# Kernel optimization log

Measured on AMD Instinct MI355X. Metric: run time of the kernel, lower is better.

The kernel has to match this reference:

```python
import jax, jax.numpy as jnp
import numpy as np

H = 64
HD = H // 2
N_PACKET = 8192
N_ROUTER = 16384
N_CHANNEL = 65536
E_PASS = 65536
N_CLASSES = 11  # pred_exp_max - pred_exp_min
NUM_MP = 2


def setup_inputs() -> dict:
    key = jax.random.key(0)
    ks = iter(jax.random.split(key, 32))

    def W(shape):
        return jax.random.normal(next(ks), shape, dtype=jnp.float32) * 0.02

    inp = {}
    # node features
    inp["freq"] = jax.random.uniform(next(ks), (N_PACKET, 1), dtype=jnp.float32)
    inp["flit"] = jax.random.normal(next(ks), (N_PACKET, 32), dtype=jnp.float32)
    inp["op_type"] = jax.random.normal(next(ks), (N_ROUTER, 4), dtype=jnp.float32)
    inp["bandwidth"] = jax.random.uniform(next(ks), (N_CHANNEL, 1), dtype=jnp.float32)
    # hetero edges: 'output' router->channel, 'input' channel->router, 'pass' packet->channel
    inp["out_src"] = jax.random.randint(next(ks), (N_CHANNEL,), 0, N_ROUTER, dtype=jnp.int32)
    inp["out_dst"] = jnp.arange(N_CHANNEL, dtype=jnp.int32)
    inp["in_src"] = jnp.arange(N_CHANNEL, dtype=jnp.int32)
    inp["in_dst"] = jax.random.randint(next(ks), (N_CHANNEL,), 0, N_ROUTER, dtype=jnp.int32)
    inp["pass_src"] = jax.random.randint(next(ks), (E_PASS,), 0, N_PACKET, dtype=jnp.int32)
    inp["pass_dst"] = jax.random.randint(next(ks), (E_PASS,), 0, N_CHANNEL, dtype=jnp.int32)
    # FeatureGen params
    inp["w_freq"] = W((1, H)); inp["b_freq"] = jnp.zeros((H,), jnp.float32)
    inp["w_flit"] = W((32, H)); inp["b_flit"] = jnp.zeros((H,), jnp.float32)
    inp["w_op"] = W((4, H)); inp["b_op"] = jnp.zeros((H,), jnp.float32)
    inp["w_bw"] = W((1, H)); inp["b_bw"] = jnp.zeros((H,), jnp.float32)
    inp["w_fp"] = W((2 * H, H)); inp["b_fp"] = jnp.zeros((H,), jnp.float32)
    inp["w_fr"] = W((H, H)); inp["b_fr"] = jnp.zeros((H,), jnp.float32)
    inp["w_fc"] = W((H, H)); inp["b_fc"] = jnp.zeros((H,), jnp.float32)
    # MessagePassing param
    inp["w_mp"] = W((H, H * HD)); inp["b_mp"] = jnp.zeros((H * HD,), jnp.float32)
    # prediction head (pred_layer=2 hidden linears + output)
    inp["w_h1"] = W((H, H)); inp["b_h1"] = jnp.zeros((H,), jnp.float32)
    inp["w_h2"] = W((H, H)); inp["b_h2"] = jnp.zeros((H,), jnp.float32)
    inp["w_out"] = W((H, N_CLASSES)); inp["b_out"] = jnp.zeros((N_CLASSES,), jnp.float32)
    return inp


def reference(freq, flit, op_type, bandwidth,
              out_src, out_dst, in_src, in_dst, pass_src, pass_dst,
              w_freq, b_freq, w_flit, b_flit, w_op, b_op, w_bw, b_bw,
              w_fp, b_fp, w_fr, b_fr, w_fc, b_fc, w_mp, b_mp,
              w_h1, b_h1, w_h2, b_h2, w_out, b_out):
    relu = jax.nn.relu
    seg = lambda d, i, n: jax.ops.segment_sum(d, i, num_segments=n)

    # ---- FeatureGen ----
    packet_feat = jnp.concatenate(
        [relu(freq @ w_freq + b_freq), relu(flit @ w_flit + b_flit)], axis=1) @ w_fp + b_fp
    router_feat = relu(op_type @ w_op + b_op) @ w_fr + b_fr
    channel_feat = relu(bandwidth @ w_bw + b_bw) @ w_fc + b_fc  # computed but unused, as in source

    # ---- MessagePassing (pfeat is identical every iteration -> hoisted) ----
    pfeat = (packet_feat @ w_mp + b_mp).reshape(N_PACKET, H, HD)      # [P,H,H/2]
    # 'pass' edges packet->channel: since rfeat_in/out depend only on dst,
    # sum_e pfeat[u_e]*rfeat[v] == (segment_sum pfeat)[v]*rfeat[v]
    agg_pfeat = seg(pfeat[pass_src], pass_dst, N_CHANNEL)             # [C,H,H/2]

    hidden = router_feat
    for _ in range(NUM_MP):
        rfeat_in = seg(hidden[out_src], out_dst, N_CHANNEL)           # [C,H]
        rfeat_out = seg(hidden[in_dst], in_src, N_CHANNEL)            # [C,H]
        partial_m_in = jnp.einsum('chd,ch->cd', agg_pfeat, rfeat_in)   # [C,H/2]
        partial_m_out = jnp.einsum('chd,ch->cd', agg_pfeat, rfeat_out)  # [C,H/2]
        m_in = seg(partial_m_in[in_src], in_dst, N_ROUTER)            # [R,H/2]
        m_out = seg(partial_m_out[out_dst], out_src, N_ROUTER)        # [R,H/2]
        m = jnp.concatenate([m_in, m_out], axis=1)                    # [R,H]
        hidden = relu(hidden + m)                                     # ActivateUpdater

    # ---- SumPooling readout (single graph in batch) ----
    embed = hidden.sum(axis=0, keepdims=True)                         # [1,H]
    # ---- prediction head ----
    pred = relu(relu(embed @ w_h1 + b_h1) @ w_h2 + b_h2) @ w_out + b_out  # [1,11]
    return pred
```

## Files before the change

kernel.cpp:

```cpp
#include <hip/hip_runtime.h>

#define NP 8192
#define NR 16384
#define EP 65536
#define NCLS 11

typedef unsigned short ushort_t;
typedef unsigned int uint_t;
typedef __attribute__((ext_vector_type(8))) short bf16x8;
typedef __attribute__((ext_vector_type(4))) float f32x4;

__device__ inline ushort_t bf16of(float v) {
    uint_t u = __builtin_bit_cast(uint_t, v);
    return (ushort_t)((u + 0x7FFFu + ((u >> 16) & 1u)) >> 16);
}

__global__ __launch_bounds__(256) void k_init(const float* __restrict__ w_mp, const float* __restrict__ b_mp,
                                              ushort_t* __restrict__ BpT, float* __restrict__ biasp,
                                              float* __restrict__ m, int* __restrict__ deg,
                                              float* __restrict__ embed) {
    int b = blockIdx.x;
    if (b < 512) {
        int i = b * 256 + threadIdx.x;
        int jp = i >> 6, k = i & 63;
        int d = jp >> 6, h = jp & 63;
        BpT[i] = bf16of(w_mp[(size_t)k * 2048 + h * 32 + d]);
        if (i < 2048) biasp[i] = b_mp[(i & 63) * 32 + (i >> 6)];
    } else {
        int zb = b - 512;
        int i = zb * 256 + threadIdx.x;
        ((float4*)m)[i] = make_float4(0.f, 0.f, 0.f, 0.f);
        if (zb < 8) ((int4*)deg)[zb * 256 + threadIdx.x] = make_int4(0, 0, 0, 0);
        if (zb == 8) ((float4*)embed)[threadIdx.x] = make_float4(0.f, 0.f, 0.f, 0.f);
    }
}

__global__ void k_hist(const int* __restrict__ pass_src, int* __restrict__ deg) {
    int e = blockIdx.x * 256 + threadIdx.x;
    if (e < EP) atomicAdd(&deg[pass_src[e]], 1);
}

__global__ void k_scan(const int* __restrict__ deg, int* __restrict__ off, int* __restrict__ cursor) {
    __shared__ int sums[256];
    int t = threadIdx.x;
    int local[32];
    int s = 0;
#pragma unroll
    for (int i = 0; i < 32; i++) { local[i] = s; s += deg[t * 32 + i]; }
    sums[t] = s;
    __syncthreads();
    for (int ofs = 1; ofs < 256; ofs <<= 1) {
        int u = (t >= ofs) ? sums[t - ofs] : 0;
        __syncthreads();
        sums[t] += u;
        __syncthreads();
    }
    int base = sums[t] - s;
#pragma unroll
    for (int i = 0; i < 32; i++) {
        int v = base + local[i];
        off[t * 32 + i] = v;
        cursor[t * 32 + i] = v;
    }
}

__global__ void k_scatter(const int* __restrict__ pass_src, const int* __restrict__ pass_dst,
                          const int* __restrict__ out_src, const int* __restrict__ in_dst,
                          int* __restrict__ cursor, int* __restrict__ csr_ab) {
    int e = blockIdx.x * 256 + threadIdx.x;
    if (e < EP) {
        int p = pass_src[e];
        int c = pass_dst[e];
        int a = out_src[c];
        int b = in_dst[c];
        int pos = atomicAdd(&cursor[p], 1);
        csr_ab[pos] = (a << 14) | b;
    }
}

__global__ __launch_bounds__(256) void k_feat(const float* __restrict__ freq, const float* __restrict__ flit,
                                              const float* __restrict__ w_freq, const float* __restrict__ b_freq,
                                              const float* __restrict__ w_flit, const float* __restrict__ b_flit,
                                              const float* __restrict__ w_fp, const float* __restrict__ b_fp,
                                              const float* __restrict__ op,
                                              const float* __restrict__ w_op, const float* __restrict__ b_op,
                                              const float* __restrict__ w_fr, const float* __restrict__ b_fr,
                                              ushort_t* __restrict__ pf_b, float* __restrict__ hidden) {
    __shared__ float smem[12544];
    int t = threadIdx.x;
    if (blockIdx.x < 512) {
        float* s_wfl = smem;
        float* s_wfp = smem + 2048;
        float* s_tmp = smem + 10240;
        float* s_wfq = smem + 12288;
        float* s_bfq = smem + 12352;
        float* s_bfl = smem + 12416;
        float* s_bfp = smem + 12480;
        if (t < 64) { s_wfq[t] = w_freq[t]; s_bfq[t] = b_freq[t]; s_bfl[t] = b_flit[t]; s_bfp[t] = b_fp[t]; }
        for (int i = t; i < 2048; i += 256) s_wfl[i] = w_flit[i];
        for (int i = t; i < 8192; i += 256) s_wfp[i] = w_fp[i];
        __syncthreads();
        int r0 = blockIdx.x * 16;
        for (int idx = t; idx < 16 * 128; idx += 256) {
            int row = idx >> 7, i = idx & 127;
            float v;
            if (i < 64) {
                v = s_bfq[i] + freq[r0 + row] * s_wfq[i];
            } else {
                int ii = i - 64;
                float acc = s_bfl[ii];
                const float* f = flit + (size_t)(r0 + row) * 32;
#pragma unroll 8
                for (int k = 0; k < 32; k++) acc += f[k] * s_wfl[k * 64 + ii];
                v = acc;
            }
            s_tmp[idx] = fmaxf(v, 0.f);
        }
        __syncthreads();
        for (int idx = t; idx < 16 * 64; idx += 256) {
            int row = idx >> 6, j = idx & 63;
            float acc = s_bfp[j];
            const float* tm = s_tmp + row * 128;
#pragma unroll 16
            for (int i = 0; i < 128; i++) acc += tm[i] * s_wfp[i * 64 + j];
            pf_b[(size_t)(r0 + row) * 64 + j] = bf16of(acc);
        }
    } else {
        float* s_wop = smem;
        float* s_wfr = smem + 256;
        float* s_tmp = smem + 4352;
        float* s_bop = smem + 5376;
        float* s_bfr = smem + 5440;
        if (t < 64) { s_bop[t] = b_op[t]; s_bfr[t] = b_fr[t]; }
        if (t < 256) s_wop[t] = w_op[t];
        for (int i = t; i < 4096; i += 256) s_wfr[i] = w_fr[i];
        __syncthreads();
        int r0 = (blockIdx.x - 512) * 16;
        for (int idx = t; idx < 16 * 64; idx += 256) {
            int row = idx >> 6, i = idx & 63;
            const float* o = op + (size_t)(r0 + row) * 4;
            float v = s_bop[i] + o[0] * s_wop[i] + o[1] * s_wop[64 + i] + o[2] * s_wop[128 + i] + o[3] * s_wop[192 + i];
            s_tmp[idx] = fmaxf(v, 0.f);
        }
        __syncthreads();
        for (int idx = t; idx < 16 * 64; idx += 256) {
            int row = idx >> 6, j = idx & 63;
            float acc = s_bfr[j];
            const float* tm = s_tmp + row * 64;
#pragma unroll 16
            for (int i = 0; i < 64; i++) acc += tm[i] * s_wfr[i * 64 + j];
            hidden[(size_t)(r0 + row) * 64 + j] = acc;
        }
    }
}

__global__ __launch_bounds__(256) void k_pfeat(const ushort_t* __restrict__ pf_b, const ushort_t* __restrict__ BpT,
                                               const float* __restrict__ biasp, ushort_t* __restrict__ pfeat_b) {
    int t = threadIdx.x;
    int wv = t >> 6, lane = t & 63;
    int p0 = blockIdx.x * 64 + wv * 16;
    int j0 = blockIdx.y * 128;
    int r = lane & 15, kg = lane >> 4;
    bf16x8 a0 = *(const bf16x8*)(pf_b + (size_t)(p0 + r) * 64 + kg * 8);
    bf16x8 a1 = *(const bf16x8*)(pf_b + (size_t)(p0 + r) * 64 + 32 + kg * 8);
#pragma unroll
    for (int jt = 0; jt < 8; jt++) {
        int j = j0 + jt * 16 + r;
        bf16x8 b0 = *(const bf16x8*)(BpT + (size_t)j * 64 + kg * 8);
        bf16x8 b1 = *(const bf16x8*)(BpT + (size_t)j * 64 + 32 + kg * 8);
        f32x4 acc = {0.f, 0.f, 0.f, 0.f};
        acc = __builtin_amdgcn_mfma_f32_16x16x32_bf16(a0, b0, acc, 0, 0, 0);
        acc = __builtin_amdgcn_mfma_f32_16x16x32_bf16(a1, b1, acc, 0, 0, 0);
        float bias = biasp[j];
#pragma unroll
        for (int q = 0; q < 4; q++) {
            pfeat_b[(size_t)(p0 + kg * 4 + q) * 2048 + j] = bf16of(acc[q] + bias);
        }
    }
}

__global__ __launch_bounds__(256) void k_mp(const ushort_t* __restrict__ pfeat_b, const float* __restrict__ hidden,
                                            const int* __restrict__ off, const int* __restrict__ deg,
                                            const int* __restrict__ csr_ab, float* __restrict__ m) {
    __shared__ float lds[4][16][64];
    int wv = threadIdx.x >> 6;
    int wid = __builtin_amdgcn_readfirstlane((blockIdx.x << 2) + wv);
    int lane = threadIdx.x & 63;
    int hi = lane >> 5, d = lane & 31;
    const uint4* pr = (const uint4*)(pfeat_b + (size_t)wid * 2048 + d * 64 + hi * 32);
    float preg[32];
#pragma unroll
    for (int q = 0; q < 4; q++) {
        uint4 u = pr[q];
        preg[q * 8 + 0] = __builtin_bit_cast(float, u.x << 16);
        preg[q * 8 + 1] = __builtin_bit_cast(float, u.x & 0xFFFF0000u);
        preg[q * 8 + 2] = __builtin_bit_cast(float, u.y << 16);
        preg[q * 8 + 3] = __builtin_bit_cast(float, u.y & 0xFFFF0000u);
        preg[q * 8 + 4] = __builtin_bit_cast(float, u.z << 16);
        preg[q * 8 + 5] = __builtin_bit_cast(float, u.z & 0xFFFF0000u);
        preg[q * 8 + 6] = __builtin_bit_cast(float, u.w << 16);
        preg[q * 8 + 7] = __builtin_bit_cast(float, u.w & 0xFFFF0000u);
    }
    int e0 = off[wid];
    int n = deg[wid];
    if (n <= 0) return;
    const float4* hb4 = (const float4*)hidden;

    int ridx = lane >> 2;
    int jj = ridx >> 1;
    int ab = ridx & 1;
    int qq = lane & 3;
    int elast = e0 + n - 1;

    float4 v0, v1, v2, v3;
    int pkj;
    {
        int ec = e0 + jj; if (ec > elast) ec = elast;
        pkj = csr_ab[ec];
        int row = ab ? (pkj & 16383) : (pkj >> 14);
        const float4* rp = hb4 + row * 16;
        v0 = rp[qq]; v1 = rp[qq + 4]; v2 = rp[qq + 8]; v3 = rp[qq + 12];
    }
    int ngroups = (n + 7) >> 3;
    for (int g = 0; g < ngroups; ++g) {
        *(float4*)&lds[wv][ridx][qq * 4]      = v0;
        *(float4*)&lds[wv][ridx][qq * 4 + 16] = v1;
        *(float4*)&lds[wv][ridx][qq * 4 + 32] = v2;
        *(float4*)&lds[wv][ridx][qq * 4 + 48] = v3;
        int pkcur = pkj;
        if (g + 1 < ngroups) {
            int ec = e0 + (g + 1) * 8 + jj; if (ec > elast) ec = elast;
            pkj = csr_ab[ec];
            int row = ab ? (pkj & 16383) : (pkj >> 14);
            const float4* rp = hb4 + row * 16;
            v0 = rp[qq]; v1 = rp[qq + 4]; v2 = rp[qq + 8]; v3 = rp[qq + 12];
        }
        int i0 = g * 8;
#pragma unroll
        for (int j = 0; j < 8; ++j) {
            if (i0 + j < n) {
                int pke = __shfl(pkcur, 8 * j, 64);
                int a_ = pke >> 14, b_ = pke & 16383;
                const float* ha = &lds[wv][2 * j][hi * 32];
                const float* hb = &lds[wv][2 * j + 1][hi * 32];
                float vi0 = 0, vi1 = 0, vi2 = 0, vi3 = 0, vo0 = 0, vo1 = 0, vo2 = 0, vo3 = 0;
#pragma unroll
                for (int q = 0; q < 8; q++) {
                    float4 xa = *(const float4*)(ha + q * 4);
                    float4 xb = *(const float4*)(hb + q * 4);
                    vi0 = fmaf(preg[4 * q + 0], xa.x, vi0);
                    vi1 = fmaf(preg[4 * q + 1], xa.y, vi1);
                    vi2 = fmaf(preg[4 * q + 2], xa.z, vi2);
                    vi3 = fmaf(preg[4 * q + 3], xa.w, vi3);
                    vo0 = fmaf(preg[4 * q + 0], xb.x, vo0);
                    vo1 = fmaf(preg[4 * q + 1], xb.y, vo1);
                    vo2 = fmaf(preg[4 * q + 2], xb.z, vo2);
                    vo3 = fmaf(preg[4 * q + 3], xb.w, vo3);
                }
                float vin = (vi0 + vi1) + (vi2 + vi3);
                float vout = (vo0 + vo1) + (vo2 + vo3);
                vin += __shfl_xor(vin, 32);
                vout += __shfl_xor(vout, 32);
                if (hi == 0) atomicAdd(&m[(size_t)b_ * 64 + d], vin);
                else         atomicAdd(&m[(size_t)a_ * 64 + 32 + d], vout);
            }
        }
    }
}

__global__ __launch_bounds__(256) void k_update0(float* __restrict__ hidden, float* __restrict__ m) {
    int i = blockIdx.x * 256 + threadIdx.x;
    float4* h4 = (float4*)hidden;
    float4* m4 = (float4*)m;
    float4 hv = h4[i];
    float4 mv = m4[i];
    float4 v;
    v.x = fmaxf(hv.x + mv.x, 0.f);
    v.y = fmaxf(hv.y + mv.y, 0.f);
    v.z = fmaxf(hv.z + mv.z, 0.f);
    v.w = fmaxf(hv.w + mv.w, 0.f);
    h4[i] = v;
    m4[i] = make_float4(0.f, 0.f, 0.f, 0.f);
}

__global__ __launch_bounds__(256) void k_update1(const float* __restrict__ hidden, const float* __restrict__ m,
                                                 float* __restrict__ embed) {
    int t = threadIdx.x;
    int base = blockIdx.x * 256 + t;
    const float4* h4 = (const float4*)hidden;
    const float4* m4 = (const float4*)m;
    float col[4] = {0.f, 0.f, 0.f, 0.f};
    for (int i = base; i < NR * 16; i += 128 * 256) {
        float4 hv = h4[i];
        float4 mv = m4[i];
        col[0] += fmaxf(hv.x + mv.x, 0.f);
        col[1] += fmaxf(hv.y + mv.y, 0.f);
        col[2] += fmaxf(hv.z + mv.z, 0.f);
        col[3] += fmaxf(hv.w + mv.w, 0.f);
    }
#pragma unroll
    for (int k = 0; k < 4; k++) {
        col[k] += __shfl_xor(col[k], 16);
        col[k] += __shfl_xor(col[k], 32);
    }
    __shared__ float scol[4][64];
    int w = t >> 6, lane = t & 63;
    if (lane < 16) {
#pragma unroll
        for (int k = 0; k < 4; k++) scol[w][lane * 4 + k] = col[k];
    }
    __syncthreads();
    if (t < 64) {
        atomicAdd(&embed[t * 16], scol[0][t] + scol[1][t] + scol[2][t] + scol[3][t]);
    }
}

__global__ void k_head(const float* __restrict__ embed,
                       const float* __restrict__ w_h1, const float* __restrict__ b_h1,
                       const float* __restrict__ w_h2, const float* __restrict__ b_h2,
                       const float* __restrict__ w_out, const float* __restrict__ b_out,
                       float* __restrict__ out) {
    __shared__ float e1[64], e2[64];
    int t = threadIdx.x;
    float acc = b_h1[t];
#pragma unroll 16
    for (int k = 0; k < 64; k++) acc += embed[k * 16] * w_h1[k * 64 + t];
    e1[t] = fmaxf(acc, 0.f);
    __syncthreads();
    acc = b_h2[t];
#pragma unroll 16
    for (int k = 0; k < 64; k++) acc += e1[k] * w_h2[k * 64 + t];
    e2[t] = fmaxf(acc, 0.f);
    __syncthreads();
    if (t < NCLS) {
        acc = b_out[t];
#pragma unroll 16
        for (int k = 0; k < 64; k++) acc += e2[k] * w_out[k * NCLS + t];
        out[t] = acc;
    }
}

extern "C" void kernel_launch(void* const* d_in, const int* in_sizes, int n_in,
                              void* d_out, int out_size, void* d_ws, size_t ws_size,
                              hipStream_t stream) {
    const float* freq   = (const float*)d_in[0];
    const float* flit   = (const float*)d_in[1];
    const float* op     = (const float*)d_in[2];
    const int* out_src  = (const int*)d_in[4];
    const int* in_dst   = (const int*)d_in[7];
    const int* pass_src = (const int*)d_in[8];
    const int* pass_dst = (const int*)d_in[9];
    const float* w_freq = (const float*)d_in[10];
    const float* b_freq = (const float*)d_in[11];
    const float* w_flit = (const float*)d_in[12];
    const float* b_flit = (const float*)d_in[13];
    const float* w_op   = (const float*)d_in[14];
    const float* b_op   = (const float*)d_in[15];
    const float* w_fp   = (const float*)d_in[18];
    const float* b_fp   = (const float*)d_in[19];
    const float* w_fr   = (const float*)d_in[20];
    const float* b_fr   = (const float*)d_in[21];
    const float* w_mp   = (const float*)d_in[24];
    const float* b_mp   = (const float*)d_in[25];
    const float* w_h1   = (const float*)d_in[26];
    const float* b_h1   = (const float*)d_in[27];
    const float* w_h2   = (const float*)d_in[28];
    const float* b_h2   = (const float*)d_in[29];
    const float* w_out  = (const float*)d_in[30];
    const float* b_out  = (const float*)d_in[31];
    float* out = (float*)d_out;

    char* ws = (char*)d_ws;
    ushort_t* pfeat_b  = (ushort_t*)(ws);
    float* hidden      = (float*)(ws + 33554432);
    float* m           = (float*)(ws + 37748736);
    float* embed       = (float*)(ws + 41943040);
    ushort_t* pf_b     = (ushort_t*)(ws + 41947136);
    ushort_t* BpT      = (ushort_t*)(ws + 44044288);
    float* biasp       = (float*)(ws + 44568576);
    int*   deg         = (int*)  (ws + 44576768);
    int*   off         = (int*)  (ws + 44609536);
    int*   cursor      = (int*)  (ws + 44642304);
    int*   csr_ab      = (int*)  (ws + 44675072);

    k_init<<<1536, 256, 0, stream>>>(w_mp, b_mp, BpT, biasp, m, deg, embed);

    k_hist<<<EP / 256, 256, 0, stream>>>(pass_src, deg);
    k_scan<<<1, 256, 0, stream>>>(deg, off, cursor);
    k_scatter<<<EP / 256, 256, 0, stream>>>(pass_src, pass_dst, out_src, in_dst, cursor, csr_ab);

    k_feat<<<1536, 256, 0, stream>>>(freq, flit, w_freq, b_freq, w_flit, b_flit, w_fp, b_fp,
                                     op, w_op, b_op, w_fr, b_fr, pf_b, hidden);
    k_pfeat<<<dim3(NP / 64, 16), 256, 0, stream>>>(pf_b, BpT, biasp, pfeat_b);

    k_mp<<<NP / 4, 256, 0, stream>>>(pfeat_b, hidden, off, deg, csr_ab, m);
    k_update0<<<NR * 16 / 256, 256, 0, stream>>>(hidden, m);

    k_mp<<<NP / 4, 256, 0, stream>>>(pfeat_b, hidden, off, deg, csr_ab, m);
    k_update1<<<128, 256, 0, stream>>>(hidden, m, embed);

    k_head<<<1, 64, 0, stream>>>(embed, w_h1, b_h1, w_h2, b_h2, w_out, b_out, out);
}
```

Before: 137.2 us.

## Compute message-passing contractions with bf16 MFMA over gathered hidden rows

Replaces the scalar FMA loop in k_mp, which staged fp32 hidden rows through LDS and reduced with shuffles, with bf16 MFMA 16x16x32 ops. These multiply 16 gathered router rows (8 edges times in/out) by the packet's 64x32 pfeat matrix. A bf16 copy of hidden is kept alongside fp32, written in k_feat and k_update0, so gathers load half the bytes and the LDS staging is dropped. The cost is lower precision in the hidden operand and a different per-lane atomic scatter pattern.

```diff
diff --git a/kernel.cpp b/kernel.cpp
--- a/kernel.cpp
+++ b/kernel.cpp
@@ -85,7 +85,8 @@
                                               const float* __restrict__ op,
                                               const float* __restrict__ w_op, const float* __restrict__ b_op,
                                               const float* __restrict__ w_fr, const float* __restrict__ b_fr,
-                                              ushort_t* __restrict__ pf_b, float* __restrict__ hidden) {
+                                              ushort_t* __restrict__ pf_b, float* __restrict__ hidden,
+                                              ushort_t* __restrict__ hidden_b) {
     __shared__ float smem[12544];
     int t = threadIdx.x;
     if (blockIdx.x < 512) {
@@ -150,6 +151,7 @@
 #pragma unroll 16
             for (int i = 0; i < 64; i++) acc += tm[i] * s_wfr[i * 64 + j];
             hidden[(size_t)(r0 + row) * 64 + j] = acc;
+            hidden_b[(size_t)(r0 + row) * 64 + j] = bf16of(acc);
         }
     }
 }
@@ -179,96 +181,77 @@
     }
 }
 
-__global__ __launch_bounds__(256) void k_mp(const ushort_t* __restrict__ pfeat_b, const float* __restrict__ hidden,
+__global__ __launch_bounds__(256) void k_mp(const ushort_t* __restrict__ pfeat_b, const ushort_t* __restrict__ hidden_b,
                                             const int* __restrict__ off, const int* __restrict__ deg,
                                             const int* __restrict__ csr_ab, float* __restrict__ m) {
-    __shared__ float lds[4][16][64];
     int wv = threadIdx.x >> 6;
     int wid = __builtin_amdgcn_readfirstlane((blockIdx.x << 2) + wv);
     int lane = threadIdx.x & 63;
-    int hi = lane >> 5, d = lane & 31;
-    const uint4* pr = (const uint4*)(pfeat_b + (size_t)wid * 2048 + d * 64 + hi * 32);
-    float preg[32];
-#pragma unroll
-    for (int q = 0; q < 4; q++) {
-        uint4 u = pr[q];
-        preg[q * 8 + 0] = __builtin_bit_cast(float, u.x << 16);
-        preg[q * 8 + 1] = __builtin_bit_cast(float, u.x & 0xFFFF0000u);
-        preg[q * 8 + 2] = __builtin_bit_cast(float, u.y << 16);
-        preg[q * 8 + 3] = __builtin_bit_cast(float, u.y & 0xFFFF0000u);
-        preg[q * 8 + 4] = __builtin_bit_cast(float, u.z << 16);
-        preg[q * 8 + 5] = __builtin_bit_cast(float, u.z & 0xFFFF0000u);
-        preg[q * 8 + 6] = __builtin_bit_cast(float, u.w << 16);
-        preg[q * 8 + 7] = __builtin_bit_cast(float, u.w & 0xFFFF0000u);
-    }
+    int col = lane & 15, kg = lane >> 4;
+    const ushort_t* pp = pfeat_b + (size_t)wid * 2048;
+    bf16x8 b0l = *(const bf16x8*)(pp + col * 64 + kg * 8);
+    bf16x8 b0h = *(const bf16x8*)(pp + col * 64 + 32 + kg * 8);
+    bf16x8 b1l = *(const bf16x8*)(pp + (16 + col) * 64 + kg * 8);
+    bf16x8 b1h = *(const bf16x8*)(pp + (16 + col) * 64 + 32 + kg * 8);
     int e0 = off[wid];
     int n = deg[wid];
     if (n <= 0) return;
-    const float4* hb4 = (const float4*)hidden;
-
-    int ridx = lane >> 2;
-    int jj = ridx >> 1;
-    int ab = ridx & 1;
-    int qq = lane & 3;
     int elast = e0 + n - 1;
-
-    float4 v0, v1, v2, v3;
+    int jj = col >> 1;
+    int ab = col & 1;
+
+    bf16x8 a0, a1;
     int pkj;
     {
         int ec = e0 + jj; if (ec > elast) ec = elast;
         pkj = csr_ab[ec];
         int row = ab ? (pkj & 16383) : (pkj >> 14);
-        const float4* rp = hb4 + row * 16;
-        v0 = rp[qq]; v1 = rp[qq + 4]; v2 = rp[qq + 8]; v3 = rp[qq + 12];
+        a0 = *(const bf16x8*)(hidden_b + (size_t)row * 64 + kg * 8);
+        a1 = *(const bf16x8*)(hidden_b + (size_t)row * 64 + 32 + kg * 8);
     }
     int ngroups = (n + 7) >> 3;
     for (int g = 0; g < ngroups; ++g) {
-        *(float4*)&lds[wv][ridx][qq * 4]      = v0;
-        *(float4*)&lds[wv][ridx][qq * 4 + 16] = v1;
-        *(float4*)&lds[wv][ridx][qq * 4 + 32] = v2;
-        *(float4*)&lds[wv][ridx][qq * 4 + 48] = v3;
+        bf16x8 a0c = a0, a1c = a1;
         int pkcur = pkj;
         if (g + 1 < ngroups) {
             int ec = e0 + (g + 1) * 8 + jj; if (ec > elast) ec = elast;
             pkj = csr_ab[ec];
             int row = ab ? (pkj & 16383) : (pkj >> 14);
-            const float4* rp = hb4 + row * 16;
-            v0 = rp[qq]; v1 = rp[qq + 4]; v2 = rp[qq + 8]; v3 = rp[qq + 12];
-        }
+            a0 = *(const bf16x8*)(hidden_b + (size_t)row * 64 + kg * 8);
+            a1 = *(const bf16x8*)(hidden_b + (size_t)row * 64 + 32 + kg * 8);
+        }
+        f32x4 acc0 = {0.f, 0.f, 0.f, 0.f};
+        f32x4 acc1 = {0.f, 0.f, 0.f, 0.f};
+        acc0 = __builtin_amdgcn_mfma_f32_16x16x32_bf16(a0c, b0l, acc0, 0, 0, 0);
+        acc0 = __builtin_amdgcn_mfma_f32_16x16x32_bf16(a1c, b0h, acc0, 0, 0, 0);
+        acc1 = __builtin_amdgcn_mfma_f32_16x16x32_bf16(a0c, b1l, acc1, 0, 0, 0);
+        acc1 = __builtin_amdgcn_mfma_f32_16x16x32_bf16(a1c, b1h, acc1, 0, 0, 0);
         int i0 = g * 8;
 #pragma unroll
-        for (int j = 0; j < 8; ++j) {
-            if (i0 + j < n) {
-                int pke = __shfl(pkcur, 8 * j, 64);
-                int a_ = pke >> 14, b_ = pke & 16383;
-                const float* ha = &lds[wv][2 * j][hi * 32];
-                const float* hb = &lds[wv][2 * j + 1][hi * 32];
-                float vi0 = 0, vi1 = 0, vi2 = 0, vi3 = 0, vo0 = 0, vo1 = 0, vo2 = 0, vo3 = 0;
-#pragma unroll
-                for (int q = 0; q < 8; q++) {
-                    float4 xa = *(const float4*)(ha + q * 4);
-                    float4 xb = *(const float4*)(hb + q * 4);
-                    vi0 = fmaf(preg[4 * q + 0], xa.x, vi0);
-                    vi1 = fmaf(preg[4 * q + 1], xa.y, vi1);
-                    vi2 = fmaf(preg[4 * q + 2], xa.z, vi2);
-                    vi3 = fmaf(preg[4 * q + 3], xa.w, vi3);
-                    vo0 = fmaf(preg[4 * q + 0], xb.x, vo0);
-                    vo1 = fmaf(preg[4 * q + 1], xb.y, vo1);
-                    vo2 = fmaf(preg[4 * q + 2], xb.z, vo2);
-                    vo3 = fmaf(preg[4 * q + 3], xb.w, vo3);
+        for (int q = 0; q < 4; q++) {
+            int s = kg * 4 + q;
+            int j = s >> 1;
+            int pk_e = __shfl(pkcur, s & 14);
+            bool valid = (i0 + j) < n;
+            if (q & 1) {
+                int a_ = pk_e >> 14;
+                if (valid) {
+                    atomicAdd(&m[(size_t)a_ * 64 + 32 + col], acc0[q]);
+                    atomicAdd(&m[(size_t)a_ * 64 + 48 + col], acc1[q]);
                 }
-                float vin = (vi0 + vi1) + (vi2 + vi3);
-                float vout = (vo0 + vo1) + (vo2 + vo3);
-                vin += __shfl_xor(vin, 32);
-                vout += __shfl_xor(vout, 32);
-                if (hi == 0) atomicAdd(&m[(size_t)b_ * 64 + d], vin);
-                else         atomicAdd(&m[(size_t)a_ * 64 + 32 + d], vout);
+            } else {
+                int b_ = pk_e & 16383;
+                if (valid) {
+                    atomicAdd(&m[(size_t)b_ * 64 + col], acc0[q]);
+                    atomicAdd(&m[(size_t)b_ * 64 + 16 + col], acc1[q]);
+                }
             }
         }
     }
 }
 
-__global__ __launch_bounds__(256) void k_update0(float* __restrict__ hidden, float* __restrict__ m) {
+__global__ __launch_bounds__(256) void k_update0(float* __restrict__ hidden, float* __restrict__ m,
+                                                 ushort_t* __restrict__ hidden_b) {
     int i = blockIdx.x * 256 + threadIdx.x;
     float4* h4 = (float4*)hidden;
     float4* m4 = (float4*)m;
@@ -281,6 +264,12 @@
     v.w = fmaxf(hv.w + mv.w, 0.f);
     h4[i] = v;
     m4[i] = make_float4(0.f, 0.f, 0.f, 0.f);
+    short4 hb;
+    hb.x = (short)bf16of(v.x);
+    hb.y = (short)bf16of(v.y);
+    hb.z = (short)bf16of(v.z);
+    hb.w = (short)bf16of(v.w);
+    *(short4*)(hidden_b + (size_t)i * 4) = hb;
 }
 
 __global__ __launch_bounds__(256) void k_update1(const float* __restrict__ hidden, const float* __restrict__ m,
@@ -382,6 +371,7 @@
     int*   off         = (int*)  (ws + 44609536);
     int*   cursor      = (int*)  (ws + 44642304);
     int*   csr_ab      = (int*)  (ws + 44675072);
+    ushort_t* hidden_b = (ushort_t*)(ws + 44937216);
 
     k_init<<<1536, 256, 0, stream>>>(w_mp, b_mp, BpT, biasp, m, deg, embed);
 
@@ -390,13 +380,13 @@
     k_scatter<<<EP / 256, 256, 0, stream>>>(pass_src, pass_dst, out_src, in_dst, cursor, csr_ab);
 
     k_feat<<<1536, 256, 0, stream>>>(freq, flit, w_freq, b_freq, w_flit, b_flit, w_fp, b_fp,
-                                     op, w_op, b_op, w_fr, b_fr, pf_b, hidden);
+                                     op, w_op, b_op, w_fr, b_fr, pf_b, hidden, hidden_b);
     k_pfeat<<<dim3(NP / 64, 16), 256, 0, stream>>>(pf_b, BpT, biasp, pfeat_b);
 
-    k_mp<<<NP / 4, 256, 0, stream>>>(pfeat_b, hidden, off, deg, csr_ab, m);
-    k_update0<<<NR * 16 / 256, 256, 0, stream>>>(hidden, m);
-
-    k_mp<<<NP / 4, 256, 0, stream>>>(pfeat_b, hidden, off, deg, csr_ab, m);
+    k_mp<<<NP / 4, 256, 0, stream>>>(pfeat_b, hidden_b, off, deg, csr_ab, m);
+    k_update0<<<NR * 16 / 256, 256, 0, stream>>>(hidden, m, hidden_b);
+
+    k_mp<<<NP / 4, 256, 0, stream>>>(pfeat_b, hidden_b, off, deg, csr_ab, m);
     k_update1<<<128, 256, 0, stream>>>(hidden, m, embed);
 
     k_head<<<1, 64, 0, stream>>>(embed, w_h1, b_h1, w_h2, b_h2, w_out, b_out, out);
```

New measurement: 127.7 us. 1.07x faster.
